# Performance work log

Hardware: AMD Instinct MI355X
Metric: run time of the kernel (lower is better)

Reference implementation:

```python
import jax, jax.numpy as jnp
import numpy as np
import math

B, C_IN, C_OUT, H, W = 16, 128, 128, 56, 56
K, S, P, D = 3, 1, 1, 1
PROD_KS = K * K


def _unfold(x, k, s, p, d):
    # torch.nn.functional.unfold equivalent -> (B, k*k, C, Ho*Wo)
    b, c, h, w = x.shape
    ho = (h + 2 * p - d * (k - 1) - 1) // s + 1
    wo = (w + 2 * p - d * (k - 1) - 1) // s + 1
    xp = jnp.pad(x, ((0, 0), (0, 0), (p, p), (p, p)))
    patches = [
        xp[:, :, i * d: i * d + (ho - 1) * s + 1: s, j * d: j * d + (wo - 1) * s + 1: s]
        for i in range(k) for j in range(k)
    ]
    u = jnp.stack(patches, axis=1)  # (B, K2, C, Ho, Wo)
    return u.reshape(b, k * k, c, ho * wo), ho, wo


def setup_inputs() -> dict:
    key = jax.random.key(0)
    k1, k2, k3, k4 = jax.random.split(key, 4)
    stdv = 1.0 / math.sqrt(C_IN * PROD_KS)
    x = jax.random.normal(k1, (B, C_IN, H, W), dtype=jnp.float32)
    weight = jax.random.uniform(k2, (1, PROD_KS, C_OUT, C_IN), dtype=jnp.float32,
                                minval=-stdv, maxval=stdv)
    b_k = jax.random.uniform(k3, (1, PROD_KS, 1, C_OUT, 1), dtype=jnp.float32,
                             minval=-stdv, maxval=stdv)
    bias = jax.random.uniform(k4, (C_OUT,), dtype=jnp.float32, minval=-stdv, maxval=stdv)
    return {"x": x, "weight": weight, "b_k": b_k, "bias": bias}


def reference(x, weight, b_k, bias):
    batch = x.shape[0]
    u, ho, wo = _unfold(x, K, S, P, D)          # (B, K2, C_in, L)
    inpt = u.transpose(0, 1, 3, 2)               # (B, K2, L, C_in)
    # GEMM: (B,K2,L,Cin) x (K2,Cout,Cin) -> (B,K2,L,Cout)
    out = jnp.einsum('bklc,koc->bklo', inpt, weight[0])
    bk = b_k[0, :, 0, :, 0]                      # (K2, Cout)
    # fused cos/sin contraction over kernel positions -> (B, L, Cout) each
    a = jnp.einsum('bklo,ko->blo', out, jnp.cos(bk))
    bb = jnp.einsum('bklo,ko->blo', out, jnp.sin(bk))
    eps = 1e-05
    a_gt = a > 0
    b_gt = bb > 0
    ab_eq = a_gt == b_gt
    theta = jnp.where(ab_eq, jnp.arctan(bb / (a + eps)), -jnp.arctan(a / (bb + eps)))
    pi = math.pi
    peak = jnp.where(ab_eq & a_gt, pi / 2.0,
           jnp.where(ab_eq & ~a_gt, -pi / 2.0,
           jnp.where(~ab_eq & ~b_gt, -pi, 0.0)))
    theta = peak - theta
    o = jnp.sin(theta) * a + jnp.cos(theta) * bb  # (B, L, Cout)
    o = o.transpose(0, 2, 1) + bias[None, :, None]  # (B, Cout, L)
    conv_out = o.reshape(batch, C_OUT, ho, wo)
    theta_out = (theta / pi).transpose(0, 2, 1).reshape(batch, C_OUT, ho, wo)
    return jnp.concatenate([conv_out, theta_out], axis=1)
```

## Files before the change

### kernel.cpp

```cpp
#include <hip/hip_runtime.h>
#include <hip/hip_bf16.h>
#include <math.h>

#define NB   16
#define CIN  128
#define COUT 128
#define HH   56
#define WW   56
#define LL   3136

typedef __attribute__((ext_vector_type(8))) short short8;
typedef __attribute__((ext_vector_type(16))) float f32x16;
typedef __attribute__((ext_vector_type(4))) float f32x4;
typedef __attribute__((ext_vector_type(4))) unsigned int uint4v;

#define PXT    256
#define NPXT   13
#define XC     58
#define XPLANE 7424
#define XUSH   14848
#define XUNITS 1856
#define XHALF  928
#define CPW    16
#define WS_TAP 1024
#define WS_N   9216
#define WBYTES 36864

#define XT_ROWS 62
#define XT_PLANE_USH (XT_ROWS*XC*16)
#define XT_CG_STRIDE 3682304

#define CSD_OFF 256
#define WSP_OFF 32768
#define XT_OFF  1212416
#define XT_SIZE 29458432
#define WL_OFF  (XT_OFF + XT_SIZE)

__global__ void prep_kernel(const float* __restrict__ w, const float* __restrict__ bk,
                            const float* __restrict__ x,
                            double* __restrict__ csd, unsigned short* __restrict__ wsp,
                            unsigned short* __restrict__ xt, unsigned* __restrict__ cnt) {
    int bid = blockIdx.x;
    if (bid == 0 && threadIdx.x == 0) *cnt = 0u;
    if (bid < 576) {
        int i = bid * 256 + threadIdx.x;
        if (i >= 9*COUT*CIN) return;
        int k = i / (COUT*CIN);
        int rem = i - k*(COUT*CIN);
        int oc = rem >> 7, c = rem & 127;
        double bkv = (double)bk[k*COUT + oc];
        double ck = cos(bkv), sk = sin(bkv);
        if (c == 0) {
            csd[k*COUT + oc]          = ck;
            csd[9*COUT + k*COUT + oc] = sk;
        }
        float wv = w[i];
        float fa = (float)(ck * (double)wv);
        float fb = (float)(sk * (double)wv);
        __hip_bfloat16 ah = __float2bfloat16(fa);
        __hip_bfloat16 al = __float2bfloat16(fa - __bfloat162float(ah));
        __hip_bfloat16 bh = __float2bfloat16(fb);
        __hip_bfloat16 bl = __float2bfloat16(fb - __bfloat162float(bh));
        int ocb = oc >> 5;
        int rowa = oc & 31, rowb = 32 + rowa;
        int cg = c >> 4, cp = c & 15;
        int sl = (((cp >> 3) ^ ((rowa >> 2) & 1)) << 3) | (cp & 7);
        size_t img = ((size_t)ocb*8 + cg) * (WBYTES/2);
        wsp[img + (size_t)k*WS_TAP + rowa*CPW + sl]        = *(unsigned short*)&ah;
        wsp[img + (size_t)k*WS_TAP + rowb*CPW + sl]        = *(unsigned short*)&bh;
        wsp[img + WS_N + (size_t)k*WS_TAP + rowa*CPW + sl] = *(unsigned short*)&al;
        wsp[img + WS_N + (size_t)k*WS_TAP + rowb*CPW + sl] = *(unsigned short*)&bl;
    } else {
        int i = (bid - 576) * 256 + threadIdx.x;
        if (i < 100352) {
            int c4 = i % 14; int t = i / 14;
            int row1 = t % 56; t /= 56;
            int bat = t & 15, cg = t >> 4;
            const float* xp = x + ((size_t)(bat*CIN + cg*16))*LL + row1*WW + c4*4;
            unsigned short hi[4][16], lo[4][16];
            #pragma unroll
            for (int j = 0; j < 16; j++) {
                f32x4 v = *(const f32x4*)(xp + (size_t)j*LL);
                #pragma unroll
                for (int cc = 0; cc < 4; cc++) {
                    float f = v[cc];
                    __hip_bfloat16 h = __float2bfloat16(f);
                    __hip_bfloat16 l = __float2bfloat16(f - __bfloat162float(h));
                    hi[cc][j] = *(unsigned short*)&h;
                    lo[cc][j] = *(unsigned short*)&l;
                }
            }
            size_t base = ((((size_t)cg*16 + bat)*2 + 0)*XT_ROWS + (row1+1))*XC + (c4*4 + 1);
            #pragma unroll
            for (int cc = 0; cc < 4; cc++) {
                unsigned short* dh = xt + (base + cc)*16;
                unsigned short* dl = dh + XT_PLANE_USH;
                *(uint4v*)dh       = *(const uint4v*)&hi[cc][0];
                *(uint4v*)(dh + 8) = *(const uint4v*)&hi[cc][8];
                *(uint4v*)dl       = *(const uint4v*)&lo[cc][0];
                *(uint4v*)(dl + 8) = *(const uint4v*)&lo[cc][8];
            }
        } else if (i < 218112) {
            int i2 = i - 100352;
            int unit = i2 % 460; int t = i2 / 460;
            int pl = t & 1; t >>= 1;
            int bat = t & 15, cg = t >> 4;
            int row, c58;
            if (unit < 348) {
                int zr = unit / 58; c58 = unit - zr*58;
                row = (zr == 0) ? 0 : (56 + zr);
            } else {
                int u2 = unit - 348; row = 1 + (u2 >> 1); c58 = (u2 & 1) ? 57 : 0;
            }
            size_t base = ((((size_t)cg*16 + bat)*2 + pl)*XT_ROWS + row)*XC + c58;
            uint4v zz = {0u,0u,0u,0u};
            *(uint4v*)(xt + base*16)     = zz;
            *(uint4v*)(xt + base*16 + 8) = zz;
        }
    }
}

__global__ __launch_bounds__(512, 4)
void mfma_kernel(const unsigned short* __restrict__ xt, const unsigned short* __restrict__ wsp,
                 const float* __restrict__ bias, float* __restrict__ out,
                 unsigned* __restrict__ cnt, unsigned* __restrict__ wl, unsigned cap)
{
    __shared__ __align__(16) unsigned short SM[2*XUSH];
    __shared__ float sm_bias[32];

    const int tid = threadIdx.x;
    int bid = blockIdx.x;
    int wk = (bid & 7) * 104 + (bid >> 3);
    const int ocb = wk & 3; wk >>= 2;
    const int pxt = wk % NPXT;
    const int bat = wk / NPXT;
    const int l0  = pxt * PXT;
    const int o0  = ocb * 32;
    const int yf  = l0 / WW;

    const int lane = tid & 63;
    const int n    = lane & 31;
    const int kh   = lane >> 5;
    const int wave = tid >> 6;

    if (tid < 32) sm_bias[tid] = bias[o0 + tid];

    unsigned xoff[4];
    #pragma unroll
    for (int k = 0; k < 4; k++) {
        int u = tid + 512*k;
        int uc = u < XUNITS ? u : XUNITS-1;
        int pl = uc >= XHALF ? 1 : 0;
        int rem = uc - pl*XHALF;
        int q  = rem >> 1;
        int hl = rem & 1;
        int hg = hl ^ ((q >> 2) & 1);
        int r  = q / XC;
        int c  = q - r*XC;
        xoff[k] = (unsigned)((((bat*2 + pl)*XT_ROWS + (yf + r))*XC + c)*32 + hg*16);
    }

    int p  = l0 + wave*32 + n;
    int pc = p < LL ? p : LL-1;
    int py = pc / WW, pxx = pc - py*WW;
    const int q0 = (py - yf)*XC + pxx;

    const int sw  = ((((n>>2)&1) ^ kh) << 3);
    const int iAa = n*CPW + sw;
    const int iAb = (32+n)*CPW + sw;

    f32x16 acc_a, acc_b;
    #pragma unroll
    for (int r = 0; r < 16; r++) { acc_a[r] = 0.f; acc_b[r] = 0.f; }

    const char* xtB  = (const char*)xt;
    const char* wspB = (const char*)wsp + (size_t)ocb * (8*(size_t)WBYTES);

    auto stage = [&](int bsel, int chn) {
        const char* xp = xtB + (size_t)chn * XT_CG_STRIDE;
        unsigned short* smb = &SM[bsel*XUSH];
        #pragma unroll
        for (int k = 0; k < 3; k++) {
            __builtin_amdgcn_global_load_lds(
                (const __attribute__((address_space(1))) unsigned int*)(xp + xoff[k]),
                (__attribute__((address_space(3))) unsigned int*)&smb[(wave*64 + 512*k)*8],
                16, 0, 0);
        }
        if (wave < 5)
            __builtin_amdgcn_global_load_lds(
                (const __attribute__((address_space(1))) unsigned int*)(xp + xoff[3]),
                (__attribute__((address_space(3))) unsigned int*)&smb[(1536 + wave*64)*8],
                16, 0, 0);
    };

    short8 wbuf[2][4];
    auto ldw = [&](int chn, int tap, short8* dst) {
        const char* tp = wspB + (size_t)chn*WBYTES + tap*(WS_TAP*2);
        dst[0] = *(const short8*)(tp + iAa*2);
        dst[1] = *(const short8*)(tp + iAb*2);
        dst[2] = *(const short8*)(tp + 2*WS_N + iAa*2);
        dst[3] = *(const short8*)(tp + 2*WS_N + iAb*2);
    };

    stage(0, 0);
    ldw(0, 0, wbuf[0]);
    ldw(0, 1, wbuf[1]);
    __syncthreads();

    #pragma unroll 1
    for (int ch = 0; ch < 8; ch++) {
        if (ch < 7) stage((ch+1)&1, ch+1);
        const unsigned short* smb = &SM[(ch&1)*XUSH];
        #pragma unroll
        for (int tap = 0; tap < 9; tap++) {
            const int ky = tap / 3, kx = tap - 3*ky;
            short8 Aha = wbuf[tap&1][0];
            short8 Ahb = wbuf[tap&1][1];
            short8 Ala = wbuf[tap&1][2];
            short8 Alb = wbuf[tap&1][3];
            if (tap < 7) ldw(ch, tap+2, wbuf[tap&1]);
            int q  = q0 + ky*XC + kx;
            int si = q*16 + ((kh ^ ((q>>2)&1)) << 3);
            short8 Bh = *(const short8*)&smb[si];
            short8 Bl = *(const short8*)&smb[XPLANE + si];
            __builtin_amdgcn_s_setprio(1);
            acc_a = __builtin_amdgcn_mfma_f32_32x32x16_bf16(Ala, Bh, acc_a, 0,0,0);
            acc_a = __builtin_amdgcn_mfma_f32_32x32x16_bf16(Aha, Bl, acc_a, 0,0,0);
            acc_a = __builtin_amdgcn_mfma_f32_32x32x16_bf16(Aha, Bh, acc_a, 0,0,0);
            acc_b = __builtin_amdgcn_mfma_f32_32x32x16_bf16(Alb, Bh, acc_b, 0,0,0);
            acc_b = __builtin_amdgcn_mfma_f32_32x32x16_bf16(Ahb, Bl, acc_b, 0,0,0);
            acc_b = __builtin_amdgcn_mfma_f32_32x32x16_bf16(Ahb, Bh, acc_b, 0,0,0);
            __builtin_amdgcn_s_setprio(0);
        }
        if (ch < 7) {
            ldw(ch+1, 0, wbuf[0]);
            ldw(ch+1, 1, wbuf[1]);
            __syncthreads();
        }
    }

    const float eps = 1e-05f;
    const float PIf = 3.14159265358979323846f;
    size_t obase = (size_t)bat * (2*COUT) * LL;
    const int pcol = wave*32 + n;
    const int pp = l0 + pcol;

    #pragma unroll
    for (int r = 0; r < 16; r++) {
        int row = (r & 3) + 8*(r >> 2) + 4*kh;
        float av = acc_a[r];
        float bv = acc_b[r];
        bool flag = (pp < LL) &&
                    (fabsf(av) < 1.5e-4f || (bv < 1.05e-5f && bv > -2.05e-5f));
        unsigned long long m = __ballot(flag);
        if (m) {
            int leader = (int)__ffsll((long long)m) - 1;
            unsigned base = 0;
            if (lane == leader) base = atomicAdd(cnt, (unsigned)__popcll(m));
            base = __shfl(base, leader);
            if (flag) {
                unsigned slot = base + (unsigned)__popcll(m & ((1ULL << lane) - 1ULL));
                if (slot < cap)
                    wl[slot] = ((unsigned)(bat*LL + pp) << 7) | (unsigned)(o0 + row);
            }
        }
        bool ag = av > 0.f, bg = bv > 0.f;
        bool eq = (ag == bg);
        float ratio = eq ? (bv / (av + eps)) : (av / (bv + eps));
        float at = atanf(ratio);
        float peak = eq ? (ag ? PIf*0.5f : -PIf*0.5f) : (bg ? 0.0f : -PIf);
        float th = peak - (eq ? at : -at);
        float c = 1.0f / sqrtf(1.0f + ratio*ratio);
        float t = eq ? (av + ratio*bv) : (ratio*av + bv);
        bool pos = eq ? ag : bg;
        float o = (pos ? c : -c) * t;
        if (pp < LL) {
            out[obase + (size_t)(o0+row)*LL + pp]      = o + sm_bias[row];
            out[obase + (size_t)(COUT+o0+row)*LL + pp] = th * (1.0f/PIf);
        }
    }
}

__global__ __launch_bounds__(256)
void fixup_kernel(const float* __restrict__ x, const float* __restrict__ w,
                  const double* __restrict__ csd, const float* __restrict__ bias,
                  const unsigned* __restrict__ cnt, const unsigned* __restrict__ wl,
                  unsigned cap, float* __restrict__ out) {
    const int lane   = threadIdx.x & 63;
    const int waveid = (blockIdx.x * 256 + threadIdx.x) >> 6;
    const int nwaves = gridDim.x * 4;
    unsigned nf = *cnt; if (nf > cap) nf = cap;
    const double PI = 3.14159265358979323846;

    for (unsigned u = waveid; u < nf; u += nwaves) {
        unsigned idx = wl[u];
        int oc = idx & 127;
        unsigned rest = idx >> 7;
        int bb_ = rest / LL;
        int l   = rest - bb_*LL;
        int yy  = l / WW;
        int xx  = l - yy*WW;
        const float* xb = x + (size_t)bb_ * CIN * LL;

        double pa = 0.0, pb = 0.0;
        #pragma unroll
        for (int k = 0; k < 9; k++) {
            int dy = k/3, dx = k - dy*3;
            int py = yy + dy - 1, px = xx + dx - 1;
            double pk = 0.0;
            if ((unsigned)py < HH && (unsigned)px < WW) {
                int base = py*WW + px;
                const float* wr = w + k*(COUT*CIN) + oc*CIN;
                int c = lane;
                pk  = (double)xb[(size_t)c*LL + base] * (double)wr[c];
                c = lane + 64;
                pk += (double)xb[(size_t)c*LL + base] * (double)wr[c];
            }
            pa += csd[k*COUT + oc] * pk;
            pb += csd[9*COUT + k*COUT + oc] * pk;
        }
        #pragma unroll
        for (int off = 32; off > 0; off >>= 1) {
            pa += __shfl_xor(pa, off, 64);
            pb += __shfl_xor(pb, off, 64);
        }
        if (lane == 0) {
            bool ag = pa > 0.0, bg = pb > 0.0;
            bool eq = (ag == bg);
            double th;
            if (eq) th = (ag ? PI*0.5 : -PI*0.5) - atan(pb / (pa + 1e-5));
            else    th = (bg ? 0.0 : -PI) + atan(pa / (pb + 1e-5));
            double o = sin(th)*pa + cos(th)*pb + (double)bias[oc];
            out[((size_t)bb_*(2*COUT) + oc) * LL + l]        = (float)o;
            out[((size_t)bb_*(2*COUT) + COUT + oc) * LL + l] = (float)(th / PI);
        }
    }
}

extern "C" void kernel_launch(void* const* d_in, const int* in_sizes, int n_in,
                              void* d_out, int out_size, void* d_ws, size_t ws_size,
                              hipStream_t stream) {
    const float* x    = (const float*)d_in[0];
    const float* w    = (const float*)d_in[1];
    const float* bk   = (const float*)d_in[2];
    const float* bias = (const float*)d_in[3];
    float* out = (float*)d_out;

    char* ws = (char*)d_ws;
    unsigned*       cnt = (unsigned*)ws;
    double*         csd = (double*)(ws + CSD_OFF);
    unsigned short* wsp = (unsigned short*)(ws + WSP_OFF);
    unsigned short* xt  = (unsigned short*)(ws + XT_OFF);
    unsigned*       wl  = (unsigned*)(ws + WL_OFF);
    unsigned cap = (ws_size > (size_t)WL_OFF + 4096) ? (unsigned)((ws_size - WL_OFF) / 4) : 0u;

    hipLaunchKernelGGL(prep_kernel,  dim3(1428), dim3(256), 0, stream,
                       w, bk, x, csd, wsp, xt, cnt);
    hipLaunchKernelGGL(mfma_kernel,  dim3(NB*NPXT*4), dim3(512), 0, stream,
                       xt, wsp, bias, out, cnt, wl, cap);
    hipLaunchKernelGGL(fixup_kernel, dim3(256), dim3(256), 0, stream,
                       x, w, csd, bias, cnt, wl, cap, out);
}
```

Baseline: 356.6 us.

## Stage weights through LDS and drop x double buffering

Weights for each channel group are now copied into LDS with asynchronous global-to-LDS loads and read from there, replacing the per-thread register prefetch straight from global memory. The x tile is no longer double-buffered: both x and weights are loaded into one buffer between two barriers after each channel group. This aims to cut redundant global weight traffic and register pressure. In exchange, the load latency is fully exposed between channel groups because there is no overlap with the MFMA work, and the loop now issues extra LDS reads per tap.

```diff
diff --git a/kernel.cpp b/kernel.cpp
--- a/kernel.cpp
+++ b/kernel.cpp
@@ -24,7 +24,9 @@
 #define CPW    16
 #define WS_TAP 1024
 #define WS_N   9216
+#define WUSH   18432
 #define WBYTES 36864
+#define WUNITS 2304
 
 #define XT_ROWS 62
 #define XT_PLANE_USH (XT_ROWS*XC*16)
@@ -125,7 +127,7 @@
                  const float* __restrict__ bias, float* __restrict__ out,
                  unsigned* __restrict__ cnt, unsigned* __restrict__ wl, unsigned cap)
 {
-    __shared__ __align__(16) unsigned short SM[2*XUSH];
+    __shared__ __align__(16) unsigned short SM[XUSH + WUSH];
     __shared__ float sm_bias[32];
 
     const int tid = threadIdx.x;
@@ -176,53 +178,55 @@
     const char* xtB  = (const char*)xt;
     const char* wspB = (const char*)wsp + (size_t)ocb * (8*(size_t)WBYTES);
 
-    auto stage = [&](int bsel, int chn) {
+    auto stage_x = [&](int chn) {
         const char* xp = xtB + (size_t)chn * XT_CG_STRIDE;
-        unsigned short* smb = &SM[bsel*XUSH];
         #pragma unroll
         for (int k = 0; k < 3; k++) {
             __builtin_amdgcn_global_load_lds(
                 (const __attribute__((address_space(1))) unsigned int*)(xp + xoff[k]),
-                (__attribute__((address_space(3))) unsigned int*)&smb[(wave*64 + 512*k)*8],
+                (__attribute__((address_space(3))) unsigned int*)&SM[(wave*64 + 512*k)*8],
                 16, 0, 0);
         }
         if (wave < 5)
             __builtin_amdgcn_global_load_lds(
                 (const __attribute__((address_space(1))) unsigned int*)(xp + xoff[3]),
-                (__attribute__((address_space(3))) unsigned int*)&smb[(1536 + wave*64)*8],
+                (__attribute__((address_space(3))) unsigned int*)&SM[(1536 + wave*64)*8],
                 16, 0, 0);
     };
-
-    short8 wbuf[2][4];
-    auto ldw = [&](int chn, int tap, short8* dst) {
-        const char* tp = wspB + (size_t)chn*WBYTES + tap*(WS_TAP*2);
-        dst[0] = *(const short8*)(tp + iAa*2);
-        dst[1] = *(const short8*)(tp + iAb*2);
-        dst[2] = *(const short8*)(tp + 2*WS_N + iAa*2);
-        dst[3] = *(const short8*)(tp + 2*WS_N + iAb*2);
+    auto stage_w = [&](int chn) {
+        const char* wp = wspB + (size_t)chn * (size_t)WBYTES;
+        #pragma unroll
+        for (int k = 0; k < 4; k++) {
+            __builtin_amdgcn_global_lo\
+ad_lds(
+                (const __attribute__((address_space(1))) unsigned int*)(wp + (tid + 512*k)*16),
+                (__attribute__((address_space(3))) unsigned int*)&SM[XUSH + (wave*64 + 512*k)*8],
+                16, 0, 0);
+        }
+        if (wave < 4)
+            __builtin_amdgcn_global_load_lds(
+                (const __attribute__((address_space(1))) unsigned int*)(wp + (2048 + tid)*16),
+                (__attribute__((address_space(3))) unsigned int*)&SM[XUSH + (2048 + wave*64)*8],
+                16, 0, 0);
     };
 
-    stage(0, 0);
-    ldw(0, 0, wbuf[0]);
-    ldw(0, 1, wbuf[1]);
+    stage_x(0);
+    stage_w(0);
     __syncthreads();
 
     #pragma unroll 1
     for (int ch = 0; ch < 8; ch++) {
-        if (ch < 7) stage((ch+1)&1, ch+1);
-        const unsigned short* smb = &SM[(ch&1)*XUSH];
         #pragma unroll
         for (int tap = 0; tap < 9; tap++) {
             const int ky = tap / 3, kx = tap - 3*ky;
-            short8 Aha = wbuf[tap&1][0];
-            short8 Ahb = wbuf[tap&1][1];
-            short8 Ala = wbuf[tap&1][2];
-            short8 Alb = wbuf[tap&1][3];
-            if (tap < 7) ldw(ch, tap+2, wbuf[tap&1]);
+            short8 Aha = *(const short8*)&SM[XUSH + tap*WS_TAP + iAa];
+            short8 Ahb = *(const short8*)&SM[XUSH + tap*WS_TAP + iAb];
+            short8 Ala = *(const short8*)&SM[XUSH + WS_N + tap*WS_TAP + iAa];
+            short8 Alb = *(const short8*)&SM[XUSH + WS_N + tap*WS_TAP + iAb];
             int q  = q0 + ky*XC + kx;
             int si = q*16 + ((kh ^ ((q>>2)&1)) << 3);
-            short8 Bh = *(const short8*)&smb[si];
-            short8 Bl = *(const short8*)&smb[XPLANE + si];
+            short8 Bh = *(const short8*)&SM[si];
+            short8 Bl = *(const short8*)&SM[XPLANE + si];
             __builtin_amdgcn_s_setprio(1);
             acc_a = __builtin_amdgcn_mfma_f32_32x32x16_bf16(Ala, Bh, acc_a, 0,0,0);
             acc_a = __builtin_amdgcn_mfma_f32_32x32x16_bf16(Aha, Bl, acc_a, 0,0,0);
@@ -233,8 +237,9 @@
             __builtin_amdgcn_s_setprio(0);
         }
         if (ch < 7) {
-            ldw(ch+1, 0, wbuf[0]);
-            ldw(ch+1, 1, wbuf[1]);
+            __syncthreads();
+            stage_x(ch+1);
+            stage_w(ch+1);
             __syncthreads();
         }
     }
```

Result: faster. 330.9 us (-7.2%).
